# Kernel tuning notes

Measured on AMD Instinct MI355X. Metric: run time of the kernel, lower is better.

The kernel has to match this reference:

```python
import jax, jax.numpy as jnp
import numpy as np

N = 100_000      # nodes
E = 1_600_000    # edges (avg degree 16)
F_IN = 165       # Elliptic node features
HID = 64         # hidden_units
NCLS = 2         # num_classes
NEG_SLOPE = 0.2  # PyG GATConv default


def setup_inputs() -> dict:
    key = jax.random.key(0)
    ks = jax.random.split(key, 9)
    x = jax.random.normal(ks[0], (N, F_IN), jnp.float32)
    edge_index = jax.random.randint(ks[1], (2, E), 0, N, jnp.int32)
    W1 = jax.random.normal(ks[2], (F_IN, HID), jnp.float32) / np.sqrt(F_IN)
    a1_src = jax.random.normal(ks[3], (HID,), jnp.float32) / np.sqrt(HID)
    a1_dst = jax.random.normal(ks[4], (HID,), jnp.float32) / np.sqrt(HID)
    b1 = jnp.zeros((HID,), jnp.float32)
    W2 = jax.random.normal(ks[5], (HID, NCLS), jnp.float32) / np.sqrt(HID)
    a2_src = jax.random.normal(ks[6], (NCLS,), jnp.float32) / np.sqrt(NCLS)
    a2_dst = jax.random.normal(ks[7], (NCLS,), jnp.float32) / np.sqrt(NCLS)
    b2 = jnp.zeros((NCLS,), jnp.float32)
    return {"x": x, "edge_index": edge_index, "W1": W1, "a1_src": a1_src,
            "a1_dst": a1_dst, "b1": b1, "W2": W2, "a2_src": a2_src,
            "a2_dst": a2_dst, "b2": b2}


def gat_layer(x, src, dst, W, a_s, a_d, b, n):
    # h: [N, out]; per-edge attention e_ij = LeakyReLU(a_s.h_j + a_d.h_i)
    h = x @ W
    e = jax.nn.leaky_relu((h @ a_s)[src] + (h @ a_d)[dst], NEG_SLOPE)
    # numerically stable segment softmax over incoming edges of each dst node
    emax = jax.ops.segment_max(e, dst, num_segments=n)
    ee = jnp.exp(e - jax.lax.stop_gradient(emax)[dst])
    denom = jax.ops.segment_sum(ee, dst, num_segments=n)
    alpha = ee / denom[dst]                       # [E_tot]
    out = jax.ops.segment_sum(alpha[:, None] * h[src], dst, num_segments=n)
    return out + b


def reference(x, edge_index, W1, a1_src, a1_dst, b1, W2, a2_src, a2_dst, b2):
    n = x.shape[0]
    loops = jnp.arange(n, dtype=edge_index.dtype)   # PyG add_self_loops=True
    src = jnp.concatenate([edge_index[0], loops])
    dst = jnp.concatenate([edge_index[1], loops])
    h = jax.nn.relu(gat_layer(x, src, dst, W1, a1_src, a1_dst, b1, n))
    # F.dropout(training=False) is identity in eval mode
    out = gat_layer(h, src, dst, W2, a2_src, a2_dst, b2, n)
    return out, edge_index
```

## Files before the change

### kernel.cpp

```cpp
#include <hip/hip_runtime.h>
#include <hip/hip_bf16.h>
#include <math.h>

#define N_NODES 100000
#define N_EDGES 1600000
#define F_IN 165
#define HID 64
#define SLOPE 0.2f

#define NBUCK 196
#define BSHIFT 9
#define BMASK 511
#define NBLK 256
#define CHUNK 6250
#define MSCAN (NBUCK * NBLK)

typedef short short8 __attribute__((ext_vector_type(8)));
typedef float f32x4 __attribute__((ext_vector_type(4)));

__device__ __forceinline__ float lrelu(float x) { return x > 0.f ? x : SLOPE * x; }

__device__ __forceinline__ unsigned short f2bf(float f) {
    unsigned u = __float_as_uint(f);
    u += 0x7FFFu + ((u >> 16) & 1u);
    return (unsigned short)(u >> 16);
}
__device__ __forceinline__ float bf2f(unsigned short b) {
    return __uint_as_float((unsigned)b << 16);
}

__global__ void k_wsw(const float* __restrict__ W1, unsigned short* __restrict__ Wsw) {
    int idx = blockIdx.x * 256 + threadIdx.x;
    if (idx >= 12288) return;
    int j = idx & 7;
    int r = idx >> 3;
    int n = r & 15; r >>= 4;
    int t = r & 3;  r >>= 2;
    int q = r & 3;  int c = r >> 2;
    int k = c * 32 + q * 8 + j;
    int col = t * 16 + n;
    float v = (k < F_IN) ? W1[k * HID + col] : 0.f;
    Wsw[idx] = f2bf(v);
}

#define ASTRIDE 200
__global__ __launch_bounds__(256, 4) void k_gemm1(const float* __restrict__ x,
                                                  const unsigned short* __restrict__ Wsw,
                                                  const float* __restrict__ a1s,
                                                  const float* __restrict__ a1d,
                                                  unsigned short* __restrict__ h1,
                                                  float* __restrict__ s1,
                                                  float* __restrict__ d1) {
    __shared__ unsigned short Ah[64 * ASTRIDE];
    const int tid = threadIdx.x;
    const int base = blockIdx.x * 64;

    for (int i = tid; i < 64 * 35; i += 256) {
        int nl = i / 35, kk = 165 + (i - nl * 35);
        Ah[nl * ASTRIDE + kk] = 0;
    }
    const int fbase = base * F_IN;
    const int flim = N_NODES * F_IN;
    for (int i = tid; i < (64 * F_IN) / 4; i += 256) {
        int f = fbase + i * 4;
        float vv[4];
        if (f + 4 <= flim) {
            float4 v = *(const float4*)&x[f];
            vv[0] = v.x; vv[1] = v.y; vv[2] = v.z; vv[3] = v.w;
        } else {
#pragma unroll
            for (int e = 0; e < 4; e++) vv[e] = (f + e < flim) ? x[f + e] : 0.f;
        }
#pragma unroll
        for (int e = 0; e < 4; e++) {
            int g = f + e;
            int node = g / F_IN;
            int kk = g - node * F_IN;
            Ah[(node - base) * ASTRIDE + kk] = f2bf(vv[e]);
        }
    }
    __syncthreads();

    const int lane = tid & 63;
    const int w = tid >> 6;
    const int m16 = lane & 15;
    const int q = lane >> 4;
    f32x4 acc[4];
#pragma unroll
    for (int t = 0; t < 4; t++) acc[t] = (f32x4){0.f, 0.f, 0.f, 0.f};

    const unsigned short* arow = &Ah[(w * 16 + m16) * ASTRIDE];
    const short8* Wsw8 = (const short8*)Wsw;
#pragma unroll
    for (int c = 0; c < 6; c++) {
        short8 a = *(const short8*)&arow[c * 32 + q * 8];
#pragma unroll
        for (int t = 0; t < 4; t++) {
            short8 b = Wsw8[(c * 4 + q) * 64 + t * 16 + m16];
            acc[t] = __builtin_amdgcn_mfma_f32_16x16x32_bf16(a, b, acc[t], 0, 0, 0);
        }
    }

    float as_l[4], ad_l[4];
#pragma unroll
    for (int t = 0; t < 4; t++) { as_l[t] = a1s[t * 16 + m16]; ad_l[t] = a1d[t * 16 + m16]; }
#pragma unroll
    for (int r = 0; r < 4; r++) {
        int node = base + w * 16 + q * 4 + r;
        bool ok = node < N_NODES;
        float ps = 0.f, pd = 0.f;
#pragma unroll
        for (int t = 0; t < 4; t++) {
            float v = acc[t][r];
            if (ok) h1[(size_t)node * HID + t * 16 + m16] = f2bf(v);
            ps += v * as_l[t];
            pd += v * ad_l[t];
        }
#pragma unroll
        for (int off = 1; off < 16; off <<= 1) {
            ps += __shfl_xor(ps, off);
            pd += __shfl_xor(pd, off);
        }
        if (ok && m16 == 0) { s1[node] = ps; d1[node] = pd; }
    }
}

__global__ __launch_bounds__(256) void k_hist(const int* __restrict__ ei,
                                              int* __restrict__ hist,
                                              float* __restrict__ out_edges) {
    __shared__ int h[NBUCK];
    int blk = blockIdx.x, t = threadIdx.x;
    for (int j = t; j < NBUCK; j += 256) h[j] = 0;
    __syncthreads();
    int i0 = blk * CHUNK, i1 = i0 + CHUNK;
    for (int i = i0 + t; i < i1; i += 256) {
        int s = ei[i];
        int d = ei[N_EDGES + i];
        out_edges[i] = (float)s;
        out_edges[N_EDGES + i] = (float)d;
        atomicAdd(&h[d >> BSHIFT], 1);
    }
    __syncthreads();
    for (int j = t; j < NBUCK; j += 256) hist[j * NBLK + blk] = h[j];
}

__global__ void k_scan1(int* __restrict__ a, int* __restrict__ bsum) {
    __shared__ int sd[256];
    int i = blockIdx.x * 256 + threadIdx.x;
    int v = a[i];
    sd[threadIdx.x] = v;
    __syncthreads();
    for (int off = 1; off < 256; off <<= 1) {
        int t = (threadIdx.x >= off) ? sd[threadIdx.x - off] : 0;
        __syncthreads();
        sd[threadIdx.x] += t;
        __syncthreads();
    }
    a[i] = sd[threadIdx.x] - v;
    if (threadIdx.x == 255) bsum[blockIdx.x] = sd[255];
}

__global__ void k_scan2(int* __restrict__ bsum, int nb) {
    __shared__ int sd[256];
    int t = threadIdx.x;
    int v = (t < nb) ? bsum[t] : 0;
    sd[t] = v;
    __syncthreads();
    for (int off = 1; off < 256; off <<= 1) {
        int u = (t >= off) ? sd[t - off] : 0;
        __syncthreads();
        sd[t] += u;
        __syncthreads();
    }
    if (t < nb) bsum[t] = sd[t] - v;
}

__global__ void k_scan3(int* __restrict__ a, const int* __restrict__ bsum) {
    int i = blockIdx.x * 256 + threadIdx.x;
    a[i] += bsum[blockIdx.x];
}

__global__ __launch_bounds__(256) void k_part(const int* __restrict__ ei,
                                              const int* __restrict__ off,
                                              unsigned* __restrict__ pairs) {
    __shared__ int base_s[NBUCK];
    __shared__ int cnt[NBUCK];
    int blk = blockIdx.x, t = threadIdx.x;
    for (int j = t; j < NBUCK; j += 256) {
        base_s[j] = off[j * NBLK + blk];
        cnt[j] = 0;
    }
    __syncthreads();
    int i0 = blk * CHUNK, i1 = i0 + CHUNK;
    for (int i = i0 + t; i < i1; i += 256) {
        int s = ei[i];
        int d = ei[N_EDGES + i];
        int b = d >> BSHIFT;
        int pos = base_s[b] + atomicAdd(&cnt[b], 1);
        pairs[pos] = ((unsigned)s << BSHIFT) | (unsigned)(d & BMASK);
    }
}

__global__ __launch_bounds__(512) void k_build2(const unsigned* __restrict__ pairs,
                                                const int* __restrict__ off,
                                                int* __restrict__ row_ptr,
                                                int* __restrict__ deg,
                                                int* __restrict__ csr) {
    __shared__ int hcnt[512];
    __shared__ int cur[512];
    int b = blockIdx.x, t = threadIdx.x;
    hcnt[t] = 0;
    __syncthreads();
    int rs = off[b * NBLK];
    int re = (b == NBUCK - 1) ? N_EDGES : off[(b + 1) * NBLK];
    for (int j = rs + t; j < re; j += 512)
        atomicAdd(&hcnt[pairs[j] & BMASK], 1);
    __syncthreads();
    int v = hcnt[t];
    cur[t] = v;
    __syncthreads();
    for (int o = 1; o < 512; o <<= 1) {
        int u = (t >= o) ? cur[t - o] : 0;
        __syncthreads();
        cur[t] += u;
        __syncthreads();
    }
    int excl = cur[t] - v;
    __syncthreads();
    cur[t] = rs + excl;
    int node = b * 512 + t;
    if (node < N_NODES) {
        row_ptr[node] = rs + excl;
        deg[node] = v;
    }
    __syncthreads();
    for (int j = rs + t; j < re; j += 512) {
        unsigned p = pairs[j];
        int pos = atomicAdd(&cur[p & BMASK], 1);
        csr[pos] = (int)(p >> BSHIFT);
    }
}

__global__ __launch_bounds__(256) void k_agg1(const unsigned short* __restrict__ h1,
                                              const float* __restrict__ s1,
                                              const float* __restrict__ d1,
                                              const int* __restrict__ row_ptr,
                                              const int* __restrict__ deg,
                                              const int* __restrict__ csr,
                                              const float* __restrict__ b1,
                                              const float* __restrict__ W2,
                                              const float* __restrict__ a2s,
                                              const float* __restrict__ a2d,
                                              float* __restrict__ node2) {
    int wid = (blockIdx.x * blockDim.x + threadIdx.x) >> 6;
    int lane = threadIdx.x & 63;
    if (wid >= N_NODES) return;
    int slot = lane >> 4;
    int cg = lane & 15;
    float di = d1[wid];
    float dpart = 0.f;
    float4 acc = make_float4(0.f, 0.f, 0.f, 0.f);
    int rs = row_ptr[wid], re = rs + deg[wid];
    for (int b = rs; b < re; b += 64) {
        int j = b + lane;
        int srcl = 0;
        float eel = 0.f;
        if (j < re) {
            srcl = csr[j];
            eel = __expf(lrelu(s1[srcl] + di));
        }
        int tmax = min(16, (re - b + 3) >> 2);
        for (int t = 0; t < tmax; t++) {
            int s = __shfl(srcl, t * 4 + slot);
            float ee = __shfl(eel, t * 4 + slot);
            ushort4 u = *(const ushort4*)&h1[(size_t)s * HID + cg * 4];
            dpart += ee;
            acc.x += ee * bf2f(u.x); acc.y += ee * bf2f(u.y);
            acc.z += ee * bf2f(u.z); acc.w += ee * bf2f(u.w);
        }
    }
#pragma unroll
    for (int off = 16; off < 64; off <<= 1) {
        acc.x += __shfl_xor(acc.x, off);
        acc.y += __shfl_xor(acc.y, off);
        acc.z += __shfl_xor(acc.z, off);
        acc.w += __shfl_xor(acc.w, off);
        dpart += __shfl_xor(dpart, off);
    }
    float ees = __expf(lrelu(s1[wid] + di));
    ushort4 us = *(const ushort4*)&h1[(size_t)wid * HID + cg * 4];
    float denom = dpart + ees;
    acc.x += ees * bf2f(us.x); acc.y += ees * bf2f(us.y);
    acc.z += ees * bf2f(us.z); acc.w += ees * bf2f(us.w);
    float inv = 1.f / denom;
    float4 bb = *(const float4*)&b1[cg * 4];
    float o0 = fmaxf(acc.x * inv + bb.x, 0.f);
    float o1 = fmaxf(acc.y * inv + bb.y, 0.f);
    float o2 = fmaxf(acc.z * inv + bb.z, 0.f);
    float o3 = fmaxf(acc.w * inv + bb.w, 0.f);
    float2 w0 = *(const float2*)&W2[(cg * 4 + 0) * 2];
    float2 w1 = *(const float2*)&W2[(cg * 4 + 1) * 2];
    float2 w2 = *(const float2*)&W2[(cg * 4 + 2) * 2];
    float2 w3 = *(const float2*)&W2[(cg * 4 + 3) * 2];
    float p0 = o0 * w0.x + o1 * w1.x + o2 * w2.x + o3 * w3.x;
    float p1 = o0 * w0.y + o1 * w1.y + o2 * w2.y + o3 * w3.y;
#pragma unroll
    for (int off = 1; off < 16; off <<= 1) {
        p0 += __shfl_xor(p0, off);
        p1 += __shfl_xor(p1, off);
    }
    if (lane == 0) {
        float s2 = p0 * a2s[0] + p1 * a2s[1];
        float d2 = p0 * a2d[0] + p1 * a2d[1];
        *(float4*)&node2[(size_t)wid * 4] = make_float4(p0, p1, s2, d2);
    }
}

__global__ __launch_bounds__(256) void k_agg2(const float* __restrict__ node2,
                                              const int* __restrict__ row_ptr,
                                              const int* __restrict__ deg,
                                              const int* __restrict__ csr,
                                              const float* __restrict__ b2,
                                              float* __restrict__ out) {
    int wid = (blockIdx.x * blockDim.x + threadIdx.x) >> 6;
    int lane = threadIdx.x & 63;
    int node = wid * 4 + (lane >> 4);
    int eg = lane & 15;
    if (node >= N_NODES) return;
    float4 vi = *(const float4*)&node2[(size_t)node * 4];
    float d2 = vi.w;
    float denom = 0.f, p0 = 0.f, p1 = 0.f;
    int rs = row_ptr[node], re = rs + deg[node];
    for (int j = rs + eg; j < re; j += 16) {
        int s = csr[j];
        float4 v = *(const float4*)&node2[(size_t)s * 4];
        float ee = __expf(lrelu(v.z + d2));
        denom += ee;
        p0 += ee * v.x;
        p1 += ee * v.y;
    }
#pragma unroll
    for (int off = 1; off < 16; off <<= 1) {
        denom += __shfl_xor(denom, off);
        p0 += __shfl_xor(p0, off);
        p1 += __shfl_xor(p1, off);
    }
    if (eg == 0) {
        float ee = __expf(lrelu(vi.z + d2));
        denom += ee;
        p0 += ee * vi.x;
        p1 += ee * vi.y;
        out[(size_t)node * 2 + 0] = p0 / denom + b2[0];
        out[(size_t)node * 2 + 1] = p1 / denom + b2[1];
    }
}

extern "C" void kernel_launch(void* const* d_in, const int* in_sizes, int n_in,
                              void* d_out, int out_size, void* d_ws, size_t ws_size,
                              hipStream_t stream) {
    const float* x   = (const float*)d_in[0];
    const int*   ei  = (const int*)d_in[1];
    const float* W1  = (const float*)d_in[2];
    const float* a1s = (const float*)d_in[3];
    const float* a1d = (const float*)d_in[4];
    const float* b1  = (const float*)d_in[5];
    const float* W2  = (const float*)d_in[6];
    const float* a2s = (const float*)d_in[7];
    const float* a2d = (const float*)d_in[8];
    const float* b2  = (const float*)d_in[9];
    float* out = (float*)d_out;

    unsigned short* h1 = (unsigned short*)d_ws;
    float* s1      = (float*)(h1 + (size_t)N_NODES * HID);
    float* d1      = s1 + N_NODES;
    float* node2   = d1 + N_NODES;
    int* row_ptr   = (int*)(node2 + (size_t)N_NODES * 4);
    int* deg       = row_ptr + N_NODES;
    int* off       = deg + N_NODES;
    int* bsum      = off + MSCAN + 64;
    int* csr       = bsum + 256;
    unsigned* pairs = (unsigned*)(csr + N_EDGES);
    unsigned short* Wsw = (unsigned short*)(pairs + N_EDGES);

    k_wsw<<<48, 256, 0, stream>>>(W1, Wsw);
    k_hist<<<NBLK, 256, 0, stream>>>(ei, off, out + 2 * N_NODES);
    k_gemm1<<<(N_NODES + 63) / 64, 256, 0, stream>>>(x, Wsw, a1s, a1d, h1, s1, d1);
    k_scan1<<<MSCAN / 256, 256, 0, stream>>>(off, bsum);
    k_scan2<<<1, 256, 0, stream>>>(bsum, MSCAN / 256);
    k_scan3<<<MSCAN / 256, 256, 0, stream>>>(off, bsum);
    k_part<<<NBLK, 256, 0, stream>>>(ei, off, pairs);
    k_build2<<<NBUCK, 512, 0, stream>>>(pairs, off, row_ptr, deg, csr);
    k_agg1<<<N_NODES / 4, 256, 0, stream>>>(h1, s1, d1, row_ptr, deg, csr,
                                            b1, W2, a2s, a2d, node2);
    k_agg2<<<(N_NODES + 15) / 16, 256, 0, stream>>>(node2, row_ptr, deg, csr, b2, out);
}
```

Measured before the change: 249.8 us.

## Split layer-1 attention weights into separate kernel and widen feature gathers

Adds a k_attw kernel that computes per-edge exp attention weights, packs them with source indices into a uint2 array, and precomputes the per-node denominator and self-loop weight. k_agg1 then reads the packed (src, weight) pairs and gathers 8 bf16 features per lane with 16-byte loads, processing 8 edges per wave step instead of 4. The goal is to take the exp and shuffle work off the gather loop and to raise memory-level parallelism in the aggregation. The cost is an extra kernel launch and an extra 12.8 MB pack write/read round trip.

Result: slower. 270.8 us (+8.4%).

```diff
diff --git a/kernel.cpp b/kernel.cpp
--- a/kernel.cpp
+++ b/kernel.cpp
@@ -25,9 +25,8 @@
     u += 0x7FFFu + ((u >> 16) & 1u);
     return (unsigned short)(u >> 16);
 }
-__device__ __forceinline__ float bf2f(unsigned short b) {
-    return __uint_as_float((unsigned)b << 16);
-}
+__device__ __forceinline__ float bflo(unsigned u) { return __uint_as_float(u << 16); }
+__device__ __forceinline__ float bfhi(unsigned u) { return __uint_as_float(u & 0xFFFF0000u); }
 
 __global__ void k_wsw(const float* __restrict__ W1, unsigned short* __restrict__ Wsw) {
     int idx = blockIdx.x * 256 + threadIdx.x;
@@ -241,12 +240,43 @@
     }
 }
 
-__global__ __launch_bounds__(256) void k_agg1(const unsigned short* __restrict__ h1,
+__global__ __launch_bounds__(256) void k_attw(const int* __restrict__ csr,
                                               const float* __restrict__ s1,
                                               const float* __restrict__ d1,
                                               const int* __restrict__ row_ptr,
                                               const int* __restrict__ deg,
-                                              const int* __restrict__ csr,
+                                              uint2* __restrict__ pack,
+                                              float* __restrict__ denom,
+                                              float* __restrict__ wself) {
+    int wid = (blockIdx.x * blockDim.x + threadIdx.x) >> 6;
+    int lane = threadIdx.x & 63;
+    int node = wid * 4 + (lane >> 4);
+    int eg = lane & 15;
+    if (node >= N_NODES) return;
+    float d = d1[node];
+    float acc = 0.f;
+    int rs = row_ptr[node], re = rs + deg[node];
+    for (int j = rs + eg; j < re; j += 16) {
+        int s = csr[j];
+        float ee = __expf(lrelu(s1[s] + d));
+        pack[j] = make_uint2((unsigned)s, __float_as_uint(ee));
+        acc += ee;
+    }
+#pragma unroll
+    for (int off = 1; off < 16; off <<= 1) acc += __shfl_xor(acc, off);
+    if (eg == 0) {
+        float se = __expf(lrelu(s1[node] + d));
+        denom[node] = acc + se;
+        wself[node] = se;
+    }
+}
+
+__global__ __launch_bounds__(256) void k_agg1(const unsigned short* __restrict__ h1,
+                                              const uint2* __restrict__ pack,
+                                              const int* __restrict__ row_ptr,
+                                              const int* __restrict__ deg,
+                                              const float* __restrict__ denom,
+                                              const float* __restrict__ wself,
                                               const float* __restrict__ b1,
                                               const float* __restrict__ W2,
                                               const float* __restrict__ a2s,
@@ -255,57 +285,56 @@
     int wid = (blockIdx.x * blockDim.x + threadIdx.x) >> 6;
     int lane = threadIdx.x & 63;
     if (wid >= N_NODES) return;
-    int slot = lane >> 4;
-    int cg = lane & 15;
-    float di = d1[wid];
-    float dpart = 0.f;
-    float4 acc = make_float4(0.f, 0.f, 0.f, 0.f);
+    int slot = lane >> 3;
+    int cg = lane & 7;
+    float acc[8];
+#pragma unroll
+    for (int c = 0; c < 8; c++) acc[c] = 0.f;
     int rs = row_ptr[wid], re = rs + deg[wid];
-    for (int b = rs; b < re; b += 64) {
-        int j = b + lane;
-        int srcl = 0;
-        float eel = 0.f;
-        if (j < re) {
-            srcl = csr[j];
-            eel = __expf(lrelu(s1[srcl] + di));
-        }
-        int tmax = min(16, (re - b + 3) >> 2);
-        for (int t = 0; t < tmax; t++) {
-            int s = __shfl(srcl, t * 4 + slot);
-            float ee = __shfl(eel, t * 4 + slot);
-            ushort4 u = *(const ushort4*)&h1[(size_t)s * HID + cg * 4];
-            dpart += ee;
-            acc.x += ee * bf2f(u.x); acc.y += ee * bf2f(u.y);
-            acc.z += ee * bf2f(u.z); acc.w += ee * bf2f(u.w);
-        }
-    }
-#pragma unroll
-    for (int off = 16; off < 64; off <<= 1) {
-        acc.x += __shfl_xor(acc.x, off);
-        acc.y += __shfl_xor(acc.y, off);
-        acc.z += __shfl_xor(acc.z, off);
-        acc.w += __shfl_xor(acc.w, off);
-        dpart += __shfl_xor(dpart, off);
-    }
-    float ees = __expf(lrelu(s1[wid] + di));
-    ushort4 us = *(const ushort4*)&h1[(size_t)wid * HID + cg * 4];
-    float denom = dpart + ees;
-    acc.x += ees * bf2f(us.x); acc.y += ees * bf2f(us.y);
-    acc.z += ees * bf2f(us.z); acc.w += ees * bf2f(us.w);
-    float inv = 1.f / denom;
-    float4 bb = *(const float4*)&b1[cg * 4];
-    float o0 = fmaxf(acc.x * inv + bb.x, 0.f);
-    float o1 = fmaxf(acc.y * inv + bb.y, 0.f);
-    float o2 = fmaxf(acc.z * inv + bb.z, 0.f);
-    float o3 = fmaxf(acc.w * inv + bb.w, 0.f);
-    float2 w0 = *(const float2*)&W2[(cg * 4 + 0) * 2];
-    float2 w1 = *(const float2*)&W2[(cg * 4 + 1) * 2];
-    float2 w2 = *(const float2*)&W2[(cg * 4 + 2) * 2];
-    float2 w3 = *(const float2*)&W2[(cg * 4 + 3) * 2];
-    float p0 = o0 * w0.x + o1 * w1.x + o2 * w2.x + o3 * w3.x;
-    float p1 = o0 * w0.y + o1 * w1.y + o2 * w2.y + o3 * w3.y;
-#pragma unroll
-    for (int off = 1; off < 16; off <<= 1) {
+    for (int j = rs + slot; j < re; j += 8) {
+        uint2 pk = pack[j];
+        float ee = __uint_as_float(pk.y);
+        uint4 u = *(const uint4*)&h1[((size_t)pk.x << 6) + cg * 8];
+        acc[0] += ee * bflo(u.x); acc[1] += ee * bfhi(u.x);
+        acc[2] += ee * bflo(u.y); acc[3] += ee * bfhi(u.y);
+        acc[4] += ee * bflo(u.z); acc[5] += ee * bfhi(u.z);
+        acc[6] += ee * bflo(u.w); acc[7] += ee * bfhi(u.w);
+    }
+#pragma unroll
+    for (int off = 8; off < 64; off <<= 1)
+#pragma unroll
+        for (int c = 0; c < 8; c++) acc[c] += __shfl_xor(acc[c], off);
+
+    float ws = wself[wid];
+    uint4 us = *(const uint4*)&h1[((size_t)wid << 6) + cg * 8];
+    acc[0] += ws * bflo(us.x); acc[1] += ws * bfhi(us.x);
+    acc[2] += ws * bflo(us.y); acc[3] += ws * bfhi(us.y);
+    acc[4] += ws * bflo(us.z); acc[5] += ws * bfhi(us.z);
+    acc[6] += ws * bflo(us.w); acc[7] += ws * bfhi(us.w);
+
+    float inv = 1.f / denom[wid];
+    float4 b0 = *(const float4*)&b1[cg * 8];
+    float4 b4 = *(const float4*)&b1[cg * 8 + 4];
+    float o[8];
+    o[0] = fmaxf(acc[0] * inv + b0.x, 0.f);
+    o[1] = fmaxf(acc[1] * inv + b0.y, 0.f);
+    o[2] = fmaxf(acc[2] * inv + b0.z, 0.f);
+    o[3] = fmaxf(acc[3] * inv + b0.w, 0.f);
+    o[4] = fmaxf(acc[4] * inv + b4.x, 0.f);
+    o[5] = fmaxf(acc[5] * inv + b4.y, 0.f);
+    o[6] = fmaxf(acc[6] * inv + b4.z, 0.f);
+    o[7] = fmaxf(acc[7] * inv + b4.w, 0.f);
+
+    float4 w01 = *(const float4*)&W2[cg * 16];
+    float4 w23 = *(const float4*)&W2[cg * 16 + 4];
+    float4 w45 = *(const float4*)&W2[cg * 16 + 8];
+    float4 w67 = *(const float4*)&W2[cg * 16 + 12];
+    float p0 = o[0] * w01.x + o[1] * w01.z + o[2] * w23.x + o[3] * w23.z
+             + o[4] * w45.x + o[5] * w45.z + o[6] * w67.x + o[7] * w67.z;
+    float p1 = o[0] * w01.y + o[1] * w01.w + o[2] * w23.y + o[3] * w23.w
+             + o[4] * w45.y + o[5] * w45.w + o[6] * w67.y + o[7] * w67.w;
+#pragma unroll
+    for (int off = 1; off < 8; off <<= 1) {
         p0 += __shfl_xor(p0, off);
         p1 += __shfl_xor(p1, off);
     }
@@ -319,7 +348,7 @@
 __global__ __launch_bounds__(256) void k_agg2(const float* __restrict__ node2,
                                               const int* __restrict__ row_ptr,
                                               const int* __restrict__ deg,
-                                              const int* __restrict__ csr,
+                                              const uint2* __restrict__ pack,
                                               const float* __restrict__ b2,
                                               float* __restrict__ out) {
     int wid = (blockIdx.x * blockDim.x + threadIdx.x) >> 6;
@@ -332,7 +361,7 @@
     float denom = 0.f, p0 = 0.f, p1 = 0.f;
     int rs = row_ptr[node], re = rs + deg[node];
     for (int j = rs + eg; j < re; j += 16) {
-        int s = csr[j];
+        int s = (int)pack[j].x;
         float4 v = *(const float4*)&node2[(size_t)s * 4];
         float ee = __expf(lrelu(v.z + d2));
         denom += ee;
@@ -374,13 +403,16 @@
     float* s1      = (float*)(h1 + (size_t)N_NODES * HID);
     float* d1      = s1 + N_NODES;
     float* node2   = d1 + N_NODES;
-    int* row_ptr   = (int*)(node2 + (size_t)N_NODES * 4);
+    float* denom   = node2 + (size_t)N_NODES * 4;
+    float* wself   = denom + N_NODES;
+    int* row_ptr   = (int*)(wself + N_NODES);
     int* deg       = row_ptr + N_NODES;
     int* off       = deg + N_NODES;
     int* bsum      = off + MSCAN + 64;
     int* csr       = bsum + 256;
     unsigned* pairs = (unsigned*)(csr + N_EDGES);
-    unsigned short* Wsw = (unsigned short*)(pairs + N_EDGES);
+    uint2* pack    = (uint2*)(pairs + N_EDGES);
+    unsigned short* Wsw = (unsigned short*)(pack + N_EDGES);
 
     k_wsw<<<48, 256, 0, stream>>>(W1, Wsw);
     k_hist<<<NBLK, 256, 0, stream>>>(ei, off, out + 2 * N_NODES);
@@ -390,7 +422,9 @@
     k_scan3<<<MSCAN / 256, 256, 0, stream>>>(off, bsum);
     k_part<<<NBLK, 256, 0, stream>>>(ei, off, pairs);
     k_build2<<<NBUCK, 512, 0, stream>>>(pairs, off, row_ptr, deg, csr);
-    k_agg1<<<N_NODES / 4, 256, 0, stream>>>(h1, s1, d1, row_ptr, deg, csr,
+    k_attw<<<(N_NODES + 15) / 16, 256, 0, stream>>>(csr, s1, d1, row_ptr, deg,
+                                                    pack, denom, wself);
+    k_agg1<<<N_NODES / 4, 256, 0, stream>>>(h1, pack, row_ptr, deg, denom, wself,
                                             b1, W2, a2s, a2d, node2);
-    k_agg2<<<(N_NODES + 15) / 16, 256, 0, stream>>>(node2, row_ptr, deg, csr, b2, out);
-}
+    k_agg2<<<(N_NODES + 15) / 16, 256, 0, stream>>>(node2, row_ptr, deg, pack, b2, out);
+}
```
